# Optimization experiments

Measured on AMD Instinct MI355X. Metric: run time of the kernel, lower is better.

## Reference

```python
import jax, jax.numpy as jnp
import numpy as np

B, N, C, OUT = 8, 2048, 128, 128

def setup_inputs() -> dict:
    key = jax.random.key(0)
    k1, k2, k3, k4, k5, k6 = jax.random.split(key, 6)
    x = jax.random.normal(k1, (B, N, C), dtype=jnp.float32)
    adj = jax.random.randint(k2, (B, N, N), 0, 2, dtype=jnp.int32)
    # fc: Linear(2*C, 1) + Sigmoid  (per-edge attention on concat(x_j, x_k))
    W_fc = jax.random.normal(k3, (2 * C, 1), dtype=jnp.float32) / np.sqrt(2 * C)
    b_fc = jax.random.normal(k4, (1,), dtype=jnp.float32) * 0.01
    # linear: Linear(C, OUT)
    W_lin = jax.random.normal(k5, (C, OUT), dtype=jnp.float32) / np.sqrt(C)
    b_lin = jax.random.normal(k6, (OUT,), dtype=jnp.float32) * 0.01
    return {"x": x, "adj": adj, "W_fc": W_fc, "b_fc": b_fc, "W_lin": W_lin, "b_lin": b_lin}

def reference(x, adj, W_fc, b_fc, W_lin, b_lin):
    # mode == 'global'
    # a_jk = sigmoid(W_fc . concat(x_j, x_k) + b_fc) where adj[j,k]==1, else 0.
    # Split the concat linear: score = (x_j . w1) + (x_k . w2) + b.
    Cdim = x.shape[-1]
    w1, w2 = W_fc[:Cdim, 0], W_fc[Cdim:, 0]
    sj = jnp.einsum('bnc,c->bn', x, w1)  # contribution of source node j
    sk = jnp.einsum('bnc,c->bn', x, w2)  # contribution of neighbor k
    scores = jax.nn.sigmoid(sj[:, :, None] + sk[:, None, :] + b_fc[0])  # [B,N,N]
    w = jnp.where(adj == 1, scores, jnp.float32(0))
    # row-normalize (divide each row by its sum)
    w = w / jnp.sum(w, axis=-1, keepdims=True)
    support = jnp.einsum('bjk,bkc->bjc', w, x)   # weighted aggregate
    return support @ W_lin + b_lin              # output projection
```

## Files before the change

### kernel.cpp

```cpp
#include <hip/hip_runtime.h>
#include <stdint.h>

#define BB 8
#define NN 2048
#define CC 128
#define OO 128

typedef __attribute__((ext_vector_type(8))) short bf16x8;
typedef __attribute__((ext_vector_type(4))) float f32x4;
typedef __attribute__((ext_vector_type(4))) int i32x4;
typedef __attribute__((ext_vector_type(4))) unsigned short u16x4;
typedef unsigned int u32;
typedef unsigned short u16;

__device__ __forceinline__ u16 f2bf(float f) {
    union { float f; u32 u; } v; v.f = f;
    u32 r = v.u + 0x7FFFu + ((v.u >> 16) & 1u);
    return (u16)(r >> 16);
}

__device__ __forceinline__ void gl_lds16(const u16* g, u16* l) {
    __builtin_amdgcn_global_load_lds(
        (__attribute__((address_space(1))) void*)(uintptr_t)g,
        (__attribute__((address_space(3))) void*)l, 16, 0, 0);
}

__global__ __launch_bounds__(256) void wt_kernel(
    const float* __restrict__ W_lin, u16* __restrict__ Wt)
{
    __shared__ float ws2[8][132];
    const int t = threadIdx.x, o0 = blockIdx.x * 8;
    f32x4 v = *(const f32x4*)(W_lin + (t >> 1) * OO + o0 + (t & 1) * 4);
    #pragma unroll
    for (int e = 0; e < 4; ++e) ws2[(t & 1) * 4 + e][t >> 1] = v[e];
    __syncthreads();
    const int oo = t >> 5, c0 = (t & 31) * 4;
    f32x4 u = *(const f32x4*)&ws2[oo][c0];
    u16x4 h;
    #pragma unroll
    for (int e = 0; e < 4; ++e) h[e] = f2bf(u[e]);
    *(u16x4*)(Wt + (size_t)(o0 + oo) * CC + c0) = h;
}

__global__ __launch_bounds__(256) void precompute_kernel(
    const float* __restrict__ x, const float* __restrict__ W_fc,
    const float* __restrict__ b_fc, const u16* __restrict__ Wt,
    float* __restrict__ sj, float* __restrict__ sk, u16* __restrict__ Yt)
{
    const int t = threadIdx.x, l = t & 63, w = t >> 6;
    const int sl = l & 15, g = l >> 4;
    const int b  = blockIdx.x >> 6;
    const int k0 = (blockIdx.x & 63) << 5;
    const int mt = w & 1, nb = (w >> 1) << 2;
    const int row = k0 + mt * 16 + sl;
    const float* xr = x + ((size_t)(b * NN + row) << 7);

    bf16x8 a[4];
    float p1 = 0.f, p2 = 0.f;
    #pragma unroll
    for (int ks = 0; ks < 4; ++ks) {
        f32x4 lo4 = *(const f32x4*)(xr + ks * 32 + g * 8);
        f32x4 hi4 = *(const f32x4*)(xr + ks * 32 + g * 8 + 4);
        f32x4 w1l = *(const f32x4*)(W_fc + ks * 32 + g * 8);
        f32x4 w1h = *(const f32x4*)(W_fc + ks * 32 + g * 8 + 4);
        f32x4 w2l = *(const f32x4*)(W_fc + CC + ks * 32 + g * 8);
        f32x4 w2h = *(const f32x4*)(W_fc + CC + ks * 32 + g * 8 + 4);
        bf16x8 av;
        #pragma unroll
        for (int e = 0; e < 4; ++e) {
            p1 += lo4[e] * w1l[e] + hi4[e] * w1h[e];
            p2 += lo4[e] * w2l[e] + hi4[e] * w2h[e];
            av[e]     = (short)f2bf(lo4[e]);
            av[e + 4] = (short)f2bf(hi4[e]);
        }
        a[ks] = av;
    }
    p1 += __shfl_xor(p1, 16); p1 += __shfl_xor(p1, 32);
    p2 += __shfl_xor(p2, 16); p2 += __shfl_xor(p2, 32);
    if (w < 2 && g == 0) {
        sj[b * NN + row] = p1 + b_fc[0];
        sk[b * NN + row] = p2;
    }

    f32x4 acc[4];
    #pragma unroll
    for (int i = 0; i < 4; ++i) acc[i] = (f32x4){0.f, 0.f, 0.f, 0.f};
    #pragma unroll
    for (int i = 0; i < 4; ++i) {
        const u16* wp = Wt + (size_t)((nb + i) * 16 + sl) * CC;
        #pragma unroll
        for (int ks = 0; ks < 4; ++ks) {
            bf16x8 bv = *(const bf16x8*)(wp + ks * 32 + g * 8);
            acc[i] = __builtin_amdgcn_mfma_f32_16x16x32_bf16(a[ks], bv, acc[i], 0, 0, 0);
        }
    }
    #pragma unroll
    for (int i = 0; i < 4; ++i) {
        const int o = (nb + i) * 16 + sl;
        u16x4 h;
        #pragma unroll
        for (int e = 0; e < 4; ++e) h[e] = f2bf(acc[i][e]);
        *(u16x4*)(Yt + (size_t)(b * OO + o) * NN + k0 + mt * 16 + g * 4) = h;
    }
}

__global__ __launch_bounds__(256, 2) void graphconv_main(
    const int* __restrict__ adj, const float* __restrict__ sj,
    const float* __restrict__ sk, const u16* __restrict__ Yt,
    const float* __restrict__ b_lin, float* __restrict__ out)
{
    __shared__ __align__(16) u16 ybuf[2][16384];
    __shared__ __align__(16) u16 pbuf[2][4096];
    float* Sld = (float*)&pbuf[0][0];

    const int t  = threadIdx.x;
    const int l  = t & 63, w = t >> 6;
    const int sw = l & 15, kg = l >> 4;
    const int lo = l & 31, hi = l >> 5;
    const int b  = blockIdx.x & 7;
    const int j0 = (blockIdx.x >> 3) << 5;

    const int* arow[4];
    float sjr[4];
    #pragma unroll
    for (int q = 0; q < 4; ++q) {
        const int R = j0 + w * 8 + 2 * q + hi;
        arow[q] = adj + ((size_t)b * NN + R) * NN + lo * 4;
        sjr[q]  = sj[b * NN + R];
    }
    const float* skp = sk + b * NN + lo * 4;

    u32 yoff[8];
    #pragma unroll
    for (int i = 0; i < 8; ++i) {
        int u  = (w * 8 + i) * 64 + l;
        int o  = u >> 4;
        int kc = (u & 15) ^ (o & 15);
        yoff[i] = (u32)(b * OO + o) * NN + kc * 8;
    }

    f32x4 acc[2][2];
    #pragma unroll
    for (int js = 0; js < 2; ++js)
        #pragma unroll
        for (int os = 0; os < 2; ++os) acc[js][os] = (f32x4){0.f, 0.f, 0.f, 0.f};
    float psum[4] = {0.f, 0.f, 0.f, 0.f};

#define SIGP(AV, SV, PAR)                                                     \
    {                                                                         \
        u16x4 hq[4];                                                          \
        _Pragma("unroll")                                                     \
        for (int q = 0; q < 4; ++q) {                                         \
            _Pragma("unroll")                                                 \
            for (int e = 0; e < 4; ++e) {                                     \
                float z  = sjr[q] + SV[e];                                    \
                float sg = __builtin_amdgcn_rcpf(1.0f + __expf(-z));          \
                float pv = AV[q][e] ? sg : 0.0f;                              \
                psum[q] += pv;                                                \
                hq[q][e] = f2bf(pv);                                          \
            }                                                                 \
        }                                                                     \
        const int kc_ = lo >> 1, hh_ = lo & 1;                                \
        _Pragma("unroll")                                                     \
        for (int q = 0; q < 4; ++q) {                                         \
            const int R = w * 8 + 2 * q + hi;                                 \
            const int u = R * 16 + (kc_ ^ (R & 15));                          \
            *(u16x4*)&pbuf[PAR][u * 8 + hh_ * 4] = hq[q];                     \
        }                                                                     \
    }

    #pragma unroll
    for (int i = 0; i < 8; ++i)
        gl_lds16(Yt + yoff[i], &ybuf[0][(w * 8 + i) * 512]);
    i32x4 aT[4], aE[4], aO[4];
    f32x4 sT, sE, sO;
    #pragma unroll
    for (int q = 0; q < 4; ++q) aT[q] = *(const i32x4*)(arow[q]);
    sT = *(const f32x4*)(skp);
    #pragma unroll
    for (int q = 0; q < 4; ++q) aE[q] = *(const i32x4*)(arow[q] + 128);
    sE = *(const f32x4*)(skp + 128);
    #pragma unroll
    for (int q = 0; q < 4; ++q) aO[q] = *(const i32x4*)(arow[q] + 256);
    sO = *(const f32x4*)(skp + 256);
    SIGP(aT, sT, 0)
    asm volatile("s_waitcnt lgkmcnt(0)" ::: "memory");
    __builtin_amdgcn_s_barrier();
    asm volatile("" ::: "memory");

#define TILE_BODY(T, AC, SC)                                                  \
    {                                                                         \
        const int T_ = (T);                                                   \
        const int tn = T_ + 1;                                                \
        const int tp = (T_ + 3 > 15) ? 15 : T_ + 3;                           \
        const int pn = tn & 1, pc = T_ & 1;                                   \
        _Pragma("unroll")                                                     \
        for (int i = 0; i < 8; ++i)                                           \
            gl_lds16(Yt + yoff[i] + (tn << 7), &ybuf[pn][(w * 8 + i) * 512]); \
        SIGP(AC, SC, pn)                                                      \
        _Pragma("unroll")                                                     \
        for (int q = 0; q < 4; ++q)                                           \
            AC[q] = *(const i32x4*)(arow[q] + tp * 128);                      \
        SC = *(const f32x4*)(skp + tp * 128);                                 \
        asm volatile("s_waitcnt vmcnt(18)" ::: "memory");                     \
        _Pragma("unroll")                                                     \
        for (int kk = 0; kk < 4; ++kk) {                                      \
            const int kc = kk * 4 + kg;                                       \
            bf16x8 af[2], bfr[2];                                             \
            _Pragma("unroll")                                                 \
            for (int js = 0; js < 2; ++js)                                    \
                af[js] = *(const bf16x8*)&pbuf[pc][((js * 16 + sw) * 16 + (kc ^ sw)) * 8]; \
            _Pragma("unroll")                                                 \
            for (int os = 0; os < 2; ++os) {                                  \
                int o = w * 32 + os * 16 + sw;                                \
                bfr[os] = *(const bf16x8*)&ybuf[pc][(o * 16 + (kc ^ sw)) * 8]; \
            }                                                                 \
            _Pragma("unroll")                                                 \
            for (int js = 0; js < 2; ++js)                                    \
                _Pragma("unroll")                                             \
                for (int os = 0; os < 2; ++os)                                \
                    acc[js][os] = __builtin_amdgcn_mfma_f32_16x16x32_bf16(    \
                        af[js], bfr[os], acc[js][os], 0, 0, 0);               \
        }                                                                     \
        asm volatile("s_waitcnt lgkmcnt(0)" ::: "memory");                    \
        __builtin_amdgcn_s_barrier();                                         \
        asm volatile("" ::: "memory");                                        \
    }

    for (int m = 0; m < 7; ++m) {
        TILE_BODY(2 * m,     aE, sE)
        TILE_BODY(2 * m + 1, aO, sO)
    }
    TILE_BODY(14, aE, sE)
#undef TILE_BODY
#undef SIGP

    asm volatile("s_waitcnt vmcnt(0)" ::: "memory");
    #pragma unroll
    for (int kk = 0; kk < 4; ++kk) {
        const int kc = kk * 4 + kg;
        bf16x8 af[2], bfr[2];
        #pragma unroll
        for (int js = 0; js < 2; ++js)
            af[js] = *(const bf16x8*)&pbuf[1][((js * 16 + sw) * 16 + (kc ^ sw)) * 8];
        #pragma unroll
        for (int os = 0; os < 2; ++os) {
            int o = w * 32 + os * 16 + sw;
            bfr[os] = *(const bf16x8*)&ybuf[1][(o * 16 + (kc ^ sw)) * 8];
        }
        #pragma unroll
        for (int js = 0; js < 2; ++js)
            #pragma unroll
            for (int os = 0; os < 2; ++os)
                acc[js][os] = __builtin_amdgcn_mfma_f32_16x16x32_bf16(
                    af[js], bfr[os], acc[js][os], 0, 0, 0);
    }

    #pragma unroll
    for (int q = 0; q < 4; ++q) {
        float s = psum[q];
        s += __shfl_xor(s, 1); s += __shfl_xor(s, 2); s += __shfl_xor(s, 4);
        s += __shfl_xor(s, 8); s += __shfl_xor(s, 16);
        if (lo == 0) Sld[w * 8 + 2 * q + hi] = s;
    }
    __syncthreads();

    #pragma unroll
    for (int js = 0; js < 2; ++js) {
        float rinv[4];
        #pragma unroll
        for (int i = 0; i < 4; ++i) rinv[i] = 1.0f / Sld[js * 16 + kg * 4 + i];
        #pragma unroll
        for (int os = 0; os < 2; ++os) {
            const int col = w * 32 + os * 16 + sw;
            const float bl = b_lin[col];
            #pragma unroll
            for (int i = 0; i < 4; ++i) {
                size_t row = (size_t)(b * NN + j0 + js * 16 + kg * 4 + i);
                out[row * OO + col] = acc[js][os][i] * rinv[i] + bl;
            }
        }
    }
}

extern "C" void kernel_launch(void* const* d_in, const int* in_sizes, int n_in,
                              void* d_out, int out_size, void* d_ws, size_t ws_size,
                              hipStream_t stream) {
    const float* x     = (const float*)d_in[0];
    const int*   adj   = (const int*)d_in[1];
    const float* W_fc  = (const float*)d_in[2];
    const float* b_fc  = (const float*)d_in[3];
    const float* W_lin = (const float*)d_in[4];
    const float* b_lin = (const float*)d_in[5];
    float* out = (float*)d_out;

    u16*   Yt = (u16*)d_ws;
    float* sj = (float*)((char*)d_ws + (size_t)BB * OO * NN * sizeof(u16));
    float* sk = sj + BB * NN;
    u16*   Wt = (u16*)(sk + BB * NN);

    wt_kernel<<<16, 256, 0, stream>>>(W_lin, Wt);
    precompute_kernel<<<512, 256, 0, stream>>>(x, W_fc, b_fc, Wt, sj, sk, Yt);
    graphconv_main<<<512, 256, 0, stream>>>(adj, sj, sk, Yt, b_lin, out);
}
```

Before: 48.71 us.

## Split output channels across two blocks to double grid and occupancy

```diff
diff --git a/kernel.cpp b/kernel.cpp
--- a/kernel.cpp
+++ b/kernel.cpp
@@ -104,12 +104,12 @@
     }
 }
 
-__global__ __launch_bounds__(256, 2) void graphconv_main(
+__global__ __launch_bounds__(256, 3) void graphconv_main(
     const int* __restrict__ adj, const float* __restrict__ sj,
     const float* __restrict__ sk, const u16* __restrict__ Yt,
     const float* __restrict__ b_lin, float* __restrict__ out)
 {
-    __shared__ __align__(16) u16 ybuf[2][16384];
+    __shared__ __align__(16) u16 ybuf[2][8192];
     __shared__ __align__(16) u16 pbuf[2][4096];
     float* Sld = (float*)&pbuf[0][0];
 
@@ -118,7 +118,8 @@
     const int sw = l & 15, kg = l >> 4;
     const int lo = l & 31, hi = l >> 5;
     const int b  = blockIdx.x & 7;
-    const int j0 = (blockIdx.x >> 3) << 5;
+    const int O0 = ((blockIdx.x >> 3) & 1) << 6;
+    const int j0 = (int)(blockIdx.x >> 4) << 5;
 
     const int* arow[4];
     float sjr[4];
@@ -130,20 +131,18 @@
     }
     const float* skp = sk + b * NN + lo * 4;
 
-    u32 yoff[8];
-    #pragma unroll
-    for (int i = 0; i < 8; ++i) {
-        int u  = (w * 8 + i) * 64 + l;
-        int o  = u >> 4;
-        int kc = (u & 15) ^ (o & 15);
-        yoff[i] = (u32)(b * OO + o) * NN + kc * 8;
-    }
-
-    f32x4 acc[2][2];
-    #pragma unroll
-    for (int js = 0; js < 2; ++js)
-        #pragma unroll
-        for (int os = 0; os < 2; ++os) acc[js][os] = (f32x4){0.f, 0.f, 0.f, 0.f};
+    u32 yoff[4];
+    #pragma unroll
+    for (int i = 0; i < 4; ++i) {
+        int u  = (w * 4 + i) * 64 + l;
+        int ol = u >> 4;
+        int kc = (u & 15) ^ (ol & 15);
+        yoff[i] = (u32)(b * OO + O0 + ol) * NN + kc * 8;
+    }
+
+    f32x4 acc[2];
+    #pragma unroll
+    for (int js = 0; js < 2; ++js) acc[js] = (f32x4){0.f, 0.f, 0.f, 0.f};
     float psum[4] = {0.f, 0.f, 0.f, 0.f};
 
 #define SIGP(AV, SV, PAR)                                                     \
@@ -170,8 +169,8 @@
     }
 
     #pragma unroll
-    for (int i = 0; i < 8; ++i)
-        gl_lds16(Yt + yoff[i], &ybuf[0][(w * 8 + i) * 512]);
+    for (int i = 0; i < 4; ++i)
+        gl_lds16(Yt + yoff[i], &ybuf[0][(w * 4 + i) * 512]);
     i32x4 aT[4], aE[4], aO[4];
     f32x4 sT, sE, sO;
     #pragma unroll
@@ -195,32 +194,27 @@
         const int tp = (T_ + 3 > 15) ? 15 : T_ + 3;                           \
         const int pn = tn & 1, pc = T_ & 1;                                   \
         _Pragma("unroll")                                                     \
-        for (int i = 0; i < 8; ++i)                                           \
-            gl_lds16(Yt + yoff[i] + (tn << 7), &ybuf[pn][(w * 8 + i) * 512]); \
+        for (int i = 0; i < 4; ++i)                                           \
+            gl_lds16(Yt + yoff[i] + (tn << 7), &ybuf[pn][(w * 4 + i) * 512]); \
         SIGP(AC, SC, pn)                                                      \
         _Pragma("unroll")                                                     \
         for (int q = 0; q < 4; ++q)                                           \
             AC[q] = *(const i32x4*)(arow[q] + tp * 128);                      \
         SC = *(const f32x4*)(skp + tp * 128);                                 \
-        asm volatile("s_waitcnt vmcnt(18)" ::: "memory");                     \
+        asm volatile("s_waitcnt vmcnt(9)" ::: "memory");                      \
         _Pragma("unroll")                                                     \
         for (int kk = 0; kk < 4; ++kk) {                                      \
             const int kc = kk * 4 + kg;                                       \
-            bf16x8 af[2], bfr[2];                                             \
+            bf16x8 af[2];                                                     \
             _Pragma("unroll")                                                 \
             for (int js = 0; js < 2; ++js)                                    \
                 af[js] = *(const bf16x8*)&pbuf[pc][((js * 16 + sw) * 16 + (kc ^ sw)) * 8]; \
-            _Pragma("unroll")                                                 \
-            for (int os = 0; os < 2; ++os) {                                  \
-                int o = w * 32 + os * 16 + sw;                                \
-                bfr[os] = *(const bf16x8*)&ybuf[pc][(o * 16 + (kc ^ sw)) * 8]; \
-            }                                                                 \
+            const int ol = w * 16 + sw;                                       \
+            bf16x8 bv = *(const bf16x8*)&ybuf[pc][(ol * 16 + (kc ^ sw)) * 8]; \
             _Pragma("unroll")                                                 \
             for (int js = 0; js < 2; ++js)                                    \
-                _Pragma("unroll")                                             \
-                for (int os = 0; os < 2; ++os)                                \
-                    acc[js][os] = __builtin_amdgcn_mfma_f32_16x16x32_bf16(    \
-                        af[js], bfr[os], acc[js][os], 0, 0, 0);               \
+                acc[js] = __builtin_amdgcn_mfma_f32_16x16x32_bf16(            \
+                    af[js], bv, acc[js], 0, 0, 0);                            \
         }                                                                     \
         asm volatile("s_waitcnt lgkmcnt(0)" ::: "memory");                    \
         __builtin_amdgcn_s_barrier();                                         \
@@ -239,21 +233,16 @@
     #pragma unroll
     for (int kk = 0; kk < 4; ++kk) {
         const int kc = kk * 4 + kg;
-        bf16x8 af[2], bfr[2];
+        bf16x8 af[2];
         #pragma unroll
         for (int js = 0; js < 2; ++js)
             af[js] = *(const bf16x8*)&pbuf[1][((js * 16 + sw) * 16 + (kc ^ sw)) * 8];
-        #pragma unroll
-        for (int os = 0; os < 2; ++os) {
-            int o = w * 32 + os * 16 + sw;
-            bfr[os] = *(const bf16x8*)&ybuf[1][(o * 16 + (kc ^ sw)) * 8];
-        }
+        const int ol = w * 16 + sw;
+        bf16x8 bv = *(const bf16x8*)&ybuf[1][(ol * 16 + (kc ^ sw)) * 8];
         #pragma unroll
         for (int js = 0; js < 2; ++js)
-            #pragma unroll
-            for (int os = 0; os < 2; ++os)
-                acc[js][os] = __builtin_amdgcn_mfma_f32_16x16x32_bf16(
-                    af[js], bfr[os], acc[js][os], 0, 0, 0);
+            acc[js] = __builtin_amdgcn_mfma_f32_16x16x32_bf16(
+                af[js], bv, acc[js], 0, 0, 0);
     }
 
     #pragma unroll
@@ -265,20 +254,17 @@
     }
     __syncthreads();
 
+    const int col = O0 + w * 16 + sw;
+    const float bl = b_lin[col];
     #pragma unroll
     for (int js = 0; js < 2; ++js) {
         float rinv[4];
         #pragma unroll
         for (int i = 0; i < 4; ++i) rinv[i] = 1.0f / Sld[js * 16 + kg * 4 + i];
         #pragma unroll
-        for (int os = 0; os < 2; ++os) {
-            const int col = w * 32 + os * 16 + sw;
-            const float bl = b_lin[col];
-            #pragma unroll
-            for (int i = 0; i < 4; ++i) {
-                size_t row = (size_t)(b * NN + j0 + js * 16 + kg * 4 + i);
-                out[row * OO + col] = acc[js][os][i] * rinv[i] + bl;
-            }
+        for (int i = 0; i < 4; ++i) {
+            size_t row = (size_t)(b * NN + j0 + js * 16 + kg * 4 + i);
+            out[row * OO + col] = acc[js][i] * rinv[i] + bl;
         }
     }
 }
@@ -301,5 +287,5 @@
 
     wt_kernel<<<16, 256, 0, stream>>>(W_lin, Wt);
     precompute_kernel<<<512, 256, 0, stream>>>(x, W_fc, b_fc, Wt, sj, sk, Yt);
-    graphconv_main<<<512, 256, 0, stream>>>(adj, sj, sk, Yt, b_lin, out);
-}
+    graphconv_main<<<1024, 256, 0, stream>>>(adj, sj, sk, Yt, b_lin, out);
+}
```

After: 61.92 us. +27.1%, slower.

## Split K dimension across two blocks with atomic accumulation and finalize pass

Applied to the files above, without the earlier changes.

```diff
diff --git a/kernel.cpp b/kernel.cpp
--- a/kernel.cpp
+++ b/kernel.cpp
@@ -104,31 +104,32 @@
     }
 }
 
-__global__ __launch_bounds__(256, 2) void graphconv_main(
+__global__ __launch_bounds__(256, 2) void graphconv_partial(
     const int* __restrict__ adj, const float* __restrict__ sj,
     const float* __restrict__ sk, const u16* __restrict__ Yt,
-    const float* __restrict__ b_lin, float* __restrict__ out)
+    float* __restrict__ outV, float* __restrict__ Srow)
 {
     __shared__ __align__(16) u16 ybuf[2][16384];
     __shared__ __align__(16) u16 pbuf[2][4096];
-    float* Sld = (float*)&pbuf[0][0];
 
     const int t  = threadIdx.x;
     const int l  = t & 63, w = t >> 6;
     const int sw = l & 15, kg = l >> 4;
     const int lo = l & 31, hi = l >> 5;
     const int b  = blockIdx.x & 7;
-    const int j0 = (blockIdx.x >> 3) << 5;
+    const int kh = (blockIdx.x >> 3) & 1;
+    const int j0 = (int)(blockIdx.x >> 4) << 5;
+    const int kbase = kh << 10;
 
     const int* arow[4];
     float sjr[4];
     #pragma unroll
     for (int q = 0; q < 4; ++q) {
         const int R = j0 + w * 8 + 2 * q + hi;
-        arow[q] = adj + ((size_t)b * NN + R) * NN + lo * 4;
+        arow[q] = adj + ((size_t)b * NN + R) * NN + kbase + lo * 4;
         sjr[q]  = sj[b * NN + R];
     }
-    const float* skp = sk + b * NN + lo * 4;
+    const float* skp = sk + b * NN + kbase + lo * 4;
 
     u32 yoff[8];
     #pragma unroll
@@ -136,7 +137,7 @@
         int u  = (w * 8 + i) * 64 + l;
         int o  = u >> 4;
         int kc = (u & 15) ^ (o & 15);
-        yoff[i] = (u32)(b * OO + o) * NN + kc * 8;
+        yoff[i] = (u32)(b * OO + o) * NN + kbase + kc * 8;
     }
 
     f32x4 acc[2][2];
@@ -192,7 +193,7 @@
     {                                                                         \
         const int T_ = (T);                                                   \
         const int tn = T_ + 1;                                                \
-        const int tp = (T_ + 3 > 15) ? 15 : T_ + 3;                           \
+        const int tp = (T_ + 3 > 7) ? 7 : T_ + 3;                             \
         const int pn = tn & 1, pc = T_ & 1;                                   \
         _Pragma("unroll")                                                     \
         for (int i = 0; i < 8; ++i)                                           \
@@ -227,11 +228,11 @@
         asm volatile("" ::: "memory");                                        \
     }
 
-    for (int m = 0; m < 7; ++m) {
+    for (int m = 0; m < 3; ++m) {
         TILE_BODY(2 * m,     aE, sE)
         TILE_BODY(2 * m + 1, aO, sO)
     }
-    TILE_BODY(14, aE, sE)
+    TILE_BODY(6, aE, sE)
 #undef TILE_BODY
 #undef SIGP
 
@@ -261,26 +262,37 @@
         float s = psum[q];
         s += __shfl_xor(s, 1); s += __shfl_xor(s, 2); s += __shfl_xor(s, 4);
         s += __shfl_xor(s, 8); s += __shfl_xor(s, 16);
-        if (lo == 0) Sld[w * 8 + 2 * q + hi] = s;
-    }
-    __syncthreads();
+        if (lo == 0) atomicAdd(&Srow[b * NN + j0 + w * 8 + 2 * q + hi], s);
+    }
 
     #pragma unroll
     for (int js = 0; js < 2; ++js) {
-        float rinv[4];
-        #pragma unroll
-        for (int i = 0; i < 4; ++i) rinv[i] = 1.0f / Sld[js * 16 + kg * 4 + i];
         #pragma unroll
         for (int os = 0; os < 2; ++os) {
             const int col = w * 32 + os * 16 + sw;
-            const float bl = b_lin[col];
             #pragma unroll
             for (int i = 0; i < 4; ++i) {
                 size_t row = (size_t)(b * NN + j0 + js * 16 + kg * 4 + i);
-                out[row * OO + col] = acc[js][os][i] * rinv[i] + bl;
+                atomicAdd(&outV[row * OO + col], acc[js][os][i]);
             }
         }
     }
+}
+
+__global__ __launch_bounds__(256) void finalize_kernel(
+    float* __restrict__ out, const float* __restrict__ Srow,
+    const float* __restrict__ b_lin)
+{
+    const int idx4 = blockIdx.x * 256 + threadIdx.x;
+    const int row  = idx4 >> 5;
+    const int c0   = (idx4 & 31) * 4;
+    float* p = out + (size_t)idx4 * 4;
+    f32x4 v  = *(f32x4*)p;
+    f32x4 bl = *(const f32x4*)(b_lin + c0);
+    const float rinv = 1.0f / Srow[row];
+    #pragma unroll
+    for (int e = 0; e < 4; ++e) v[e] = v[e] * rinv + bl[e];
+    *(f32x4*)p = v;
 }
 
 extern "C" void kernel_launch(void* const* d_in, const int* in_sizes, int n_in,
@@ -294,12 +306,16 @@
     const float* b_lin = (const float*)d_in[5];
     float* out = (float*)d_out;
 
-    u16*   Yt = (u16*)d_ws;
-    float* sj = (float*)((char*)d_ws + (size_t)BB * OO * NN * sizeof(u16));
-    float* sk = sj + BB * NN;
-    u16*   Wt = (u16*)(sk + BB * NN);
-
+    u16*   Yt   = (u16*)d_ws;
+    float* sj   = (float*)((char*)d_ws + (size_t)BB * OO * NN * sizeof(u16));
+    float* sk   = sj + BB * NN;
+    u16*   Wt   = (u16*)(sk + BB * NN);
+    float* Srow = (float*)(Wt + OO * CC);
+
+    hipMemsetAsync(out, 0, (size_t)out_size * sizeof(float), stream);
+    hipMemsetAsync(Srow, 0, (size_t)BB * NN * sizeof(float), stream);
     wt_kernel<<<16, 256, 0, stream>>>(W_lin, Wt);
     precompute_kernel<<<512, 256, 0, stream>>>(x, W_fc, b_fc, Wt, sj, sk, Yt);
-    graphconv_main<<<512, 256, 0, stream>>>(adj, sj, sk, Yt, b_lin, out);
-}
+    graphconv_partial<<<1024, 256, 0, stream>>>(adj, sj, sk, Yt, out, Srow);
+    finalize_kernel<<<2048, 256, 0, stream>>>(out, Srow, b_lin);
+}
```

Measured after the change: 66.03 us. 1.36x slower.
